# Optimization experiments

Hardware: AMD Instinct MI355X
Metric: run time of the kernel (lower is better)

Reference implementation:

```python
import jax, jax.numpy as jnp
import numpy as np

B, T, N, E = 4, 30, 2000, 32000
F_IN, F_HID, F_GRU, N_CLS = 8, 64, 128, 2


def setup_inputs() -> dict:
    key = jax.random.key(0)
    ks = jax.random.split(key, 12)
    return {
        "x": jax.random.normal(ks[0], (B, T, N, F_IN), jnp.float32),
        "edge_index": jax.random.randint(ks[1], (B, T, 2, E), 0, N, jnp.int32),
        "W1": jax.random.normal(ks[2], (F_IN, F_HID), jnp.float32) * 0.1,
        "b1": jax.random.normal(ks[3], (F_HID,), jnp.float32) * 0.1,
        "W2": jax.random.normal(ks[4], (F_HID, F_HID), jnp.float32) * 0.1,
        "b2": jax.random.normal(ks[5], (F_HID,), jnp.float32) * 0.1,
        "W_ih": jax.random.normal(ks[6], (3 * F_GRU, F_HID), jnp.float32) * 0.1,
        "W_hh": jax.random.normal(ks[7], (3 * F_GRU, F_GRU), jnp.float32) * 0.1,
        "b_ih": jax.random.normal(ks[8], (3 * F_GRU,), jnp.float32) * 0.1,
        "b_hh": jax.random.normal(ks[9], (3 * F_GRU,), jnp.float32) * 0.1,
        "fc_w": jax.random.normal(ks[10], (N_CLS, F_GRU), jnp.float32) * 0.1,
        "fc_b": jax.random.normal(ks[11], (N_CLS,), jnp.float32) * 0.1,
    }


def _gcn_conv(x, src, dst, W, b):
    # PyG GCNConv (edge_weight=None): add self-loops, sym-normalize, x@W, scatter-add, +bias
    n = x.shape[0]
    loops = jnp.arange(n, dtype=src.dtype)
    s = jnp.concatenate([src, loops])
    d = jnp.concatenate([dst, loops])
    deg = jax.ops.segment_sum(jnp.ones(s.shape[0], x.dtype), d, num_segments=n)
    dis = jnp.where(deg > 0, jax.lax.rsqrt(deg), 0.0)
    norm = dis[s] * dis[d]                      # [E+N]
    h = x @ W                                   # [N, Fout]
    msg = h[s] * norm[:, None]                  # gather + scale
    return jax.ops.segment_sum(msg, d, num_segments=n) + b


def _frame_embed(x, ei, W1, b1, W2, b2):
    # one graph frame -> mean-pooled 64-d embedding
    src, dst = ei[0], ei[1]
    h = jax.nn.relu(_gcn_conv(x, src, dst, W1, b1))
    h = jax.nn.relu(_gcn_conv(h, src, dst, W2, b2))
    return h.mean(axis=0)


def _gru(H, W_ih, W_hh, b_ih, b_hh):
    # H: [T, B, F_HID]; torch GRU gate order: r, z, n
    def step(h, x_t):
        gi = x_t @ W_ih.T + b_ih                # [B, 3H]
        gh = h @ W_hh.T + b_hh
        i_r, i_z, i_n = jnp.split(gi, 3, axis=-1)
        h_r, h_z, h_n = jnp.split(gh, 3, axis=-1)
        r = jax.nn.sigmoid(i_r + h_r)
        z = jax.nn.sigmoid(i_z + h_z)
        n = jnp.tanh(i_n + r * h_n)
        h_new = (1.0 - z) * n + z * h
        return h_new, None
    h0 = jnp.zeros((H.shape[1], F_GRU), H.dtype)
    h_final, _ = jax.lax.scan(step, h0, H)
    return h_final                              # [B, F_GRU]


def reference(x, edge_index, W1, b1, W2, b2, W_ih, W_hh, b_ih, b_hh, fc_w, fc_b):
    G = B * T
    xf = x.reshape(G, N, F_IN)
    eif = edge_index.reshape(G, 2, E)
    emb = jax.vmap(_frame_embed, in_axes=(0, 0, None, None, None, None))(
        xf, eif, W1, b1, W2, b2)                # [G, 64]
    H = emb.reshape(B, T, F_HID).transpose(1, 0, 2)  # [T, B, 64]
    h_final = _gru(H, W_ih, W_hh, b_ih, b_hh)   # [B, 128]
    return h_final @ fc_w.T + fc_b              # [B, 2]
```

## Files before the change

kernel.cpp:

```cpp
#include <hip/hip_runtime.h>
#include <math.h>

#define G    120
#define Nn   2000
#define Ee   32000
#define Tt   30
#define Bb   4
#define Fg   128
#define QCAP 9216
#define TSLOT 48

static __device__ __forceinline__ unsigned short f2bf(float f) {
    unsigned u = __float_as_uint(f);
    u += 0x7fffu + ((u >> 16) & 1u);
    return (unsigned short)(u >> 16);
}

#if defined(__has_builtin)
#if __has_builtin(__builtin_amdgcn_cvt_f32_fp8) && __has_builtin(__builtin_amdgcn_cvt_pk_fp8_f32)
#define HW_FP8 1
#endif
#if __has_builtin(__builtin_amdgcn_cvt_pk_f32_fp8)
#define HW_FP8_PK 1
typedef float floatx2 __attribute__((ext_vector_type(2)));
#endif
#endif

static __device__ __forceinline__ unsigned fp8_enc_sw(float x) {
    unsigned s = (__float_as_uint(x) >> 24) & 0x80u;
    float ax = fminf(fabsf(x), 448.f);
    unsigned em;
    if (ax < 0.015625f) {
        em = (unsigned)__float2int_rn(ax * 512.f);
    } else {
        int e = (int)(__float_as_uint(ax) >> 23) - 127;
        float r = ax * __uint_as_float((unsigned)((130 - e) << 23));
        int q = __float2int_rn(r);
        em = (unsigned)(((e + 7) << 3) + (q - 8));
        em = min(em, 126u);
    }
    return s | em;
}
static __device__ __forceinline__ float fp8_dec_sw(unsigned b) {
    unsigned em = b & 0x7fu;
    float mag;
    if (em < 8u) mag = (float)em * 0.001953125f;
    else mag = __uint_as_float((((em >> 3) + 120u) << 23) | ((em & 7u) << 20));
    return (b & 0x80u) ? -mag : mag;
}
static __device__ __forceinline__ unsigned fp8_pack4(float a, float b, float c, float d) {
#ifdef HW_FP8
    int w = __builtin_amdgcn_cvt_pk_fp8_f32(a, b, 0, false);
    w = __builtin_amdgcn_cvt_pk_fp8_f32(c, d, w, true);
    return (unsigned)w;
#else
    return fp8_enc_sw(a) | (fp8_enc_sw(b) << 8) | (fp8_enc_sw(c) << 16) | (fp8_enc_sw(d) << 24);
#endif
}
static __device__ __forceinline__ void fp8x4_dec(unsigned dw, float* o) {
#ifdef HW_FP8_PK
    floatx2 lo = __builtin_amdgcn_cvt_pk_f32_fp8((int)dw, false);
    floatx2 hi = __builtin_amdgcn_cvt_pk_f32_fp8((int)dw, true);
    o[0] = lo[0]; o[1] = lo[1]; o[2] = hi[0]; o[3] = hi[1];
#else
    o[0] = fp8_dec_sw(dw & 0xffu);
    o[1] = fp8_dec_sw((dw >> 8) & 0xffu);
    o[2] = fp8_dec_sw((dw >> 16) & 0xffu);
    o[3] = fp8_dec_sw((dw >> 24) & 0xffu);
#endif
}

__global__ void __launch_bounds__(1024, 1)
k_build(const int* __restrict__ ei, float* __restrict__ dis,
        int* __restrict__ startA, int* __restrict__ cntA,
        int* __restrict__ csr, unsigned* __restrict__ ellT,
        int* __restrict__ cntS, int* __restrict__ ordS,
        float* __restrict__ emb) {
    __shared__ int   hist[Nn];
    __shared__ float disl[Nn];
    __shared__ int   ws[512];
    __shared__ int   csr_l[QCAP];
    __shared__ int   cntQ[500];
    __shared__ int   exQ[500];
    __shared__ int   nodeAt[500];
    __shared__ int   dh[64];
    __shared__ int   db[64];
    __shared__ int   ovfS;
    int i = blockIdx.x;
    int xcd = i & 7;
    int j = i >> 3;
    int f15 = j >> 2;
    int q = j & 3;
    int g = xcd * 15 + f15;
    int gq = g * 4 + q;
    int lo = q * 500;
    int tid = threadIdx.x;
    for (int idx = tid; idx < Nn; idx += 1024) hist[idx] = 0;
    if (tid < 64) dh[tid] = 0;
    if (tid == 0) ovfS = 0;
    if (q == 0 && tid < 64) emb[g * 64 + tid] = 0.f;
    __syncthreads();
    const int* srcp = ei + (size_t)g * 2 * Ee;
    const int* dstp = srcp + Ee;
    for (int it = tid; it < Ee / 4; it += 1024) {
        int4 d = reinterpret_cast<const int4*>(dstp)[it];
        atomicAdd(&hist[d.x], 1);
        atomicAdd(&hist[d.y], 1);
        atomicAdd(&hist[d.z], 1);
        atomicAdd(&hist[d.w], 1);
    }
    __syncthreads();
    for (int idx = tid; idx < Nn; idx += 1024) disl[idx] = rsqrtf((float)hist[idx] + 1.0f);
    int cnt = 0;
    if (tid < 512) ws[tid] = (tid < 500) ? hist[lo + tid] : 0;
    if (tid < 500) cnt = hist[lo + tid];
    __syncthreads();
    for (int off = 1; off < 512; off <<= 1) {
        int v = 0;
        if (tid < 512 && tid >= off) v = ws[tid - off];
        __syncthreads();
        if (tid < 512) ws[tid] += v;
        __syncthreads();
    }
    int ex = 0;
    if (tid < 500) ex = ws[tid] - cnt;
    if (tid < 500) {
        hist[lo + tid] = ex;
        cntQ[tid] = cnt;
        exQ[tid] = ex;
        if (cnt > TSLOT - 1) atomicMax(&ovfS, 1);
        atomicAdd(&dh[min(cnt, 63)], 1);
    }
    __syncthreads();
    if (tid == 0) {
        int s = 0;
        for (int b = 0; b < 64; ++b) { db[b] = s; s += dh[b]; }
    }
    __syncthreads();
    if (tid < 64) dh[tid] = db[tid];
    __syncthreads();
    if (tid < 500) {
        int p = atomicAdd(&dh[min(cnt, 63)], 1);
        nodeAt[p] = tid;
    }
    for (int it = tid; it < Ee / 4; it += 1024) {
        int4 d = reinterpret_cast<const int4*>(dstp)[it];
        int4 s = reinterpret_cast<const int4*>(srcp)[it];
        if (d.x >= lo && d.x < lo + 500) { int p = atomicAdd(&hist[d.x], 1); if (p < QCAP) csr_l[p] = s.x; }
        if (d.y >= lo && d.y < lo + 500) { int p = atomicAdd(&hist[d.y], 1); if (p < QCAP) csr_l[p] = s.y; }
        if (d.z >= lo && d.z < lo + 500) { int p = atomicAdd(&hist[d.z], 1); if (p < QCAP) csr_l[p] = s.z; }
        if (d.w >= lo && d.w < lo + 500) { int p = atomicAdd(&hist[d.w], 1); if (p < QCAP) csr_l[p] = s.w; }
    }
    __syncthreads();
    if (tid < 500) {
        int n_own = lo + tid;
        size_t gn_own = (size_t)g * Nn + n_own;
        cntA[gn_own] = cnt;
        startA[gn_own] = gq * QCAP + ex;
        dis[gn_own] = disl[n_own];
        int sl = nodeAt[tid];
        int n2 = lo + sl;
        int cnt2 = cntQ[sl];
        int ex2 = exQ[sl];
        int c = q * 500 + tid;
        size_t gc = (size_t)g * Nn + c;
        cntS[gc] = cnt2;
        ordS[gc] = n2;
        float dn2 = disl[n2];
        unsigned* et = ellT + (size_t)g * TSLOT * Nn + c;
        et[0] = (unsigned)n2 | ((unsigned)f2bf(dn2 * dn2) << 16);
        int m2 = min(cnt2, TSLOT - 1);
        for (int e = 0; e < m2; ++e) {
            int s = csr_l[ex2 + e];
            et[(size_t)(e + 1) * Nn] = (unsigned)s | ((unsigned)f2bf(disl[s] * dn2) << 16);
        }
    }
    __syncthreads();
    if (ovfS) {
        int total = ws[511];
        int* cg = csr + (size_t)gq * QCAP;
        for (int it = tid; it < total; it += 1024) cg[it] = csr_l[it];
    }
}

__global__ void __launch_bounds__(256)
k_fused(const float* __restrict__ x, const unsigned* __restrict__ ellT,
        const int* __restrict__ cntS, const int* __restrict__ ordS,
        const int* __restrict__ startA, const int* __restrict__ csr,
        const float* __restrict__ dis,
        const float* __restrict__ W1, const float* __restrict__ b1,
        const float* __restrict__ W2, unsigned char* __restrict__ t2f) {
    int i = blockIdx.x;
    int xcd = i & 7;
    int j = i >> 3;
    int g = xcd * 15 + (j >> 3);
    int blk = j & 7;
    int p = blk * 256 + threadIdx.x;
    bool valid = (p < Nn);
    size_t gp = (size_t)g * Nn + (valid ? p : 0);
    int n = valid ? ordS[gp] : 0;
    int cnt = valid ? cntS[gp] : 0;
    int myc = valid ? (min(cnt, TSLOT - 1) + 1) : 0;
    float aX[8];
#pragma unroll
    for (int k = 0; k < 8; ++k) aX[k] = 0.f;
    {
        const unsigned* et = ellT + (size_t)g * TSLOT * Nn + (valid ? p : 0);
        const float4* x4 = reinterpret_cast<const float4*>(x + (size_t)g * Nn * 8);
        for (int e = 0; e < TSLOT; ++e) {
            if (!__any(e < myc)) break;
            if (e < myc) {
                unsigned u = et[(size_t)e * Nn];
                float w = __uint_as_float(u & 0xffff0000u);
                int s = u & 0xffffu;
                float4 r0 = x4[s * 2], r1 = x4[s * 2 + 1];
                aX[0] += r0.x * w; aX[1] += r0.y * w; aX[2] += r0.z * w; aX[3] += r0.w * w;
                aX[4] += r1.x * w; aX[5] += r1.y * w; aX[6] += r1.z * w; aX[7] += r1.w * w;
            }
        }
        if (cnt > TSLOT - 1) {
            size_t gn = (size_t)g * Nn + n;
            float dn = dis[gn];
            int start = startA[gn];
            const float* dsg = dis + (size_t)g * Nn;
            for (int e = TSLOT - 1; e < cnt; ++e) {
                int s = csr[start + e];
                float w = dsg[s] * dn;
                float4 r0 = x4[s * 2], r1 = x4[s * 2 + 1];
                aX[0] += r0.x * w; aX[1] += r0.y * w; aX[2] += r0.z * w; aX[3] += r0.w * w;
                aX[4] += r1.x * w; aX[5] += r1.y * w; aX[6] += r1.z * w; aX[7] += r1.w * w;
            }
        }
    }
    float h1r[64];
    {
        const float4* b14 = reinterpret_cast<const float4*>(b1);
#pragma unroll
        for (int f4 = 0; f4 < 16; ++f4) {
            float4 b = b14[f4];
            h1r[4 * f4 + 0] = b.x; h1r[4 * f4 + 1] = b.y;
            h1r[4 * f4 + 2] = b.z; h1r[4 * f4 + 3] = b.w;
        }
        const float4* W14 = reinterpret_cast<const float4*>(W1);
#pragma unroll
        for (int k = 0; k < 8; ++k) {
            float hk = aX[k];
#pragma unroll
            for (int f4 = 0; f4 < 16; ++f4) {
                float4 w = W14[k * 16 + f4];
                h1r[4 * f4 + 0] += hk * w.x; h1r[4 * f4 + 1] += hk * w.y;
                h1r[4 * f4 + 2] += hk * w.z; h1r[4 * f4 + 3] += hk * w.w;
            }
        }
#pragma unroll
        for (int f = 0; f < 64; ++f) h1r[f] = fmaxf(h1r[f], 0.f);
    }
    uint4 oh[2][2];
    {
        const float4* W24 = reinterpret_cast<const float4*>(W2);
#pragma unroll
        for (int hf = 0; hf < 2; ++hf) {
            float acch[32];
#pragma unroll
            for (int f = 0; f < 32; ++f) acch[f] = 0.f;
#pragma unroll
            for (int k = 0; k < 64; ++k) {
                float hk = h1r[k];
#pragma unroll
                for (int f4 = 0; f4 < 8; ++f4) {
                    float4 w = W24[k * 16 + hf * 8 + f4];
                    acch[4 * f4 + 0] += hk * w.x; acch[4 * f4 + 1] += hk * w.y;
                    acch[4 * f4 + 2] += hk * w.z; acch[4 * f4 + 3] += hk * w.w;
                }
            }
            oh[hf][0].x = fp8_pack4(acch[0],  acch[1],  acch[2],  acch[3]);
            oh[hf][0].y = fp8_pack4(acch[4],  acch[5],  acch[6],  acch[7]);
            oh[hf][0].z = fp8_pack4(acch[8],  acch[9],  acch[10], acch[11]);
            oh[hf][0].w = fp8_pack4(acch[12], acch[13], acch[14], acch[15]);
            oh[hf][1].x = fp8_pack4(acch[16], acch[17], acch[18], acch[19]);
            oh[hf][1].y = fp8_pack4(acch[20], acch[21], acch[22], acch[23]);
            oh[hf][1].z = fp8_pack4(acch[24], acch[25], acch[26], acch[27]);
            oh[hf][1].w = fp8_pack4(acch[28], acch[29], acch[30], acch[31]);
        }
    }
    if (valid) {
        uint4* op = reinterpret_cast<uint4*>(t2f + ((size_t)g * Nn + n) * 64);
        op[0] = oh[0][0]; op[1] = oh[0][1]; op[2] = oh[1][0]; op[3] = oh[1][1];
    }
}

__global__ void __launch_bounds__(1024, 1)
k_aggF(const unsigned char* __restrict__ t2f, const unsigned* __restrict__ ellT,
       const int* __restrict__ cntS, const int* __restrict__ ordS,
       const int* __restrict__ startA, const int* __restrict__ csr,
       const float* __restrict__ dis, const float* __restrict__ bias,
       float* __restrict__ emb) {
    __shared__ uint4 stage[Nn * 5];
    int i = blockIdx.x;
    int xcd = i & 7;
    int j = i >> 3;
    int g = xcd * 15 + (j >> 1);
    int half = j & 1;
    int tid = threadIdx.x;
    int w = tid >> 6, lane = tid & 63;
    {
        const uint4* src = reinterpret_cast<const uint4*>(t2f + (size_t)g * Nn * 64);
        for (int it = tid; it < Nn * 4; it += 1024)
            stage[(it >> 2) * 5 + (it & 3)] = src[it];
    }
    __syncthreads();
#define ROWFMA(dw, base) { float o_[4]; fp8x4_dec(dw, o_); \
    acc[base + 0] += o_[0] * wt; acc[base + 1] += o_[1] * wt; \
    acc[base + 2] += o_[2] * wt; acc[base + 3] += o_[3] * wt; }
    int po = w * 64 + lane;
    int p = half * 1000 + po;
    bool valid = (po < 1000);
    size_t gp = (size_t)g * Nn + (valid ? p : 0);
    int cnt = valid ? cntS[gp] : 0;
    int myc = valid ? (min(cnt, TSLOT - 1) + 1) : 0;
    float acc[64];
#pragma unroll
    for (int k = 0; k < 64; ++k) acc[k] = 0.f;
    const unsigned* et = ellT + (size_t)g * TSLOT * Nn + (valid ? p : 0);
    for (int e = 0; e < TSLOT; ++e) {
        if (!__any(e < myc)) break;
        if (e < myc) {
            unsigned u = et[(size_t)e * Nn];
            float wt = __uint_as_float(u & 0xffff0000u);
            int s = u & 0xffffu;
            uint4 r0 = stage[s * 5], r1 = stage[s * 5 + 1];
            uint4 r2 = stage[s * 5 + 2], r3 = stage[s * 5 + 3];
            ROWFMA(r0.x, 0)  ROWFMA(r0.y, 4)  ROWFMA(r0.z, 8)  ROWFMA(r0.w, 12)
            ROWFMA(r1.x, 16) ROWFMA(r1.y, 20) ROWFMA(r1.z, 24) ROWFMA(r1.w, 28)
            ROWFMA(r2.x, 32) ROWFMA(r2.y, 36) ROWFMA(r2.z, 40) ROWFMA(r2.w, 44)
            ROWFMA(r3.x, 48) ROWFMA(r3.y, 52) ROWFMA(r3.z, 56) ROWFMA(r3.w, 60)
        }
    }
    if (cnt > TSLOT - 1) {
        int n = ordS[gp];
        size_t gn = (size_t)g * Nn + n;
        float dn = dis[gn];
        int start = startA[gn];
        const float* dsg = dis + (size_t)g * Nn;
        for (int e = TSLOT - 1; e < cnt; ++e) {
            int s = csr[start + e];
            float wt = dsg[s] * dn;
            uint4 r0 = stage[s * 5], r1 = stage[s * 5 + 1];
            uint4 r2 = stage[s * 5 + 2], r3 = stage[s * 5 + 3];
            ROWFMA(r0.x, 0)  ROWFMA(r0.y, 4)  ROWFMA(r0.z, 8)  ROWFMA(r0.w, 12)
            ROWFMA(r1.x, 16) ROWFMA(r1.y, 20) ROWFMA(r1.z, 24) ROWFMA(r1.w, 28)
            ROWFMA(r2.x, 32) ROWFMA(r2.y, 36) ROWFMA(r2.z, 40) ROWFMA(r2.w, 44)
            ROWFMA(r3.x, 48) ROWFMA(r3.y, 52) ROWFMA(r3.z, 56) ROWFMA(r3.w, 60)
        }
    }
#undef ROWFMA
    float pool = 0.f;
#pragma unroll
    for (int k = 0; k < 64; ++k) {
        float v = valid ? fmaxf(acc[k] + bias[k], 0.f) : 0.f;
        v += __shfl_xor(v, 1);  v += __shfl_xor(v, 2);  v += __shfl_xor(v, 4);
        v += __shfl_xor(v, 8);  v += __shfl_xor(v, 16); v += __shfl_xor(v, 32);
        if (lane == k) pool = v;
    }
    atomicAdd(&emb[g * 64 + lane], pool * (1.0f / Nn));
}

__global__ void k_gi(const float* __restrict__ emb, const float* __restrict__ W_ih,
                     const float* __restrict__ b_ih, float* __restrict__ gi) {
    __shared__ float xs[64];
    int g = blockIdx.x;
    int j = threadIdx.x;
    if (j < 64) xs[j] = emb[g * 64 + j];
    __syncthreads();
    float a0 = 0.f, a1 = 0.f, a2 = 0.f, a3 = 0.f;
    const float* wr = W_ih + j * 64;
#pragma unroll
    for (int k = 0; k < 16; ++k) {
        a0 += wr[4 * k + 0] * xs[4 * k + 0];
        a1 += wr[4 * k + 1] * xs[4 * k + 1];
        a2 += wr[4 * k + 2] * xs[4 * k + 2];
        a3 += wr[4 * k + 3] * xs[4 * k + 3];
    }
    gi[(size_t)g * 384 + j] = b_ih[j] + ((a0 + a1) + (a2 + a3));
}

__global__ void __launch_bounds__(768, 1)
k_gru_seq(const float* __restrict__ gi, const float* __restrict__ W_hh,
          const float* __restrict__ b_hh, const float* __restrict__ fc_w,
          const float* __restrict__ fc_b, float* __restrict__ out) {
    __shared__ float h[Fg];
    __shared__ float part[768];
    int b = blockIdx.x;
    int tid = threadIdx.x;
    int row = tid >> 1;
    int half = tid & 1;
    float w[64];
    const float* wr = W_hh + (size_t)row * Fg + half * 64;
#pragma unroll
    for (int i = 0; i < 64; ++i) w[i] = wr[i];
    if (tid < Fg) h[tid] = 0.f;
    __syncthreads();
    for (int t = 0; t < Tt; ++t) {
        const float* hh = &h[half * 64];
        float a0 = 0.f, a1 = 0.f, a2 = 0.f, a3 = 0.f;
#pragma unroll
        for (int i = 0; i < 16; ++i) {
            a0 += w[4 * i + 0] * hh[4 * i + 0];
            a1 += w[4 * i + 1] * hh[4 * i + 1];
            a2 += w[4 * i + 2] * hh[4 * i + 2];
            a3 += w[4 * i + 3] * hh[4 * i + 3];
        }
        part[tid] = (a0 + a1) + (a2 + a3);
        __syncthreads();
        if (tid < Fg) {
            int j = tid;
            const float* gib = gi + ((size_t)b * Tt + t) * 384;
            float hr = b_hh[j]       + part[2 * j]           + part[2 * j + 1];
            float hz = b_hh[128 + j] + part[2 * (128 + j)]   + part[2 * (128 + j) + 1];
            float hn = b_hh[256 + j] + part[2 * (256 + j)]   + part[2 * (256 + j) + 1];
            float r  = 1.f / (1.f + expf(-(gib[j] + hr)));
            float z  = 1.f / (1.f + expf(-(gib[128 + j] + hz)));
            float nn = tanhf(gib[256 + j] + r * hn);
            h[j] = (1.f - z) * nn + z * h[j];
        }
        __syncthreads();
    }
    if (tid < 2) {
        float acc = fc_b[tid];
        for (int k = 0; k < Fg; ++k) acc += fc_w[tid * Fg + k] * h[k];
        out[b * 2 + tid] = acc;
    }
}

extern "C" void kernel_launch(void* const* d_in, const int* in_sizes, int n_in,
                              void* d_out, int out_size, void* d_ws, size_t ws_size,
                              hipStream_t stream) {
    const float* x     = (const float*)d_in[0];
    const int*   ei    = (const int*)  d_in[1];
    const float* W1    = (const float*)d_in[2];
    const float* b1    = (const float*)d_in[3];
    const float* W2    = (const float*)d_in[4];
    const float* b2    = (const float*)d_in[5];
    const float* W_ih  = (const float*)d_in[6];
    const float* W_hh  = (const float*)d_in[7];
    const float* b_ih  = (const float*)d_in[8];
    const float* b_hh  = (const float*)d_in[9];
    const float* fc_w  = (const float*)d_in[10];
    const float* fc_b  = (const float*)d_in[11];
    float* out = (float*)d_out;

    char* ws = (char*)d_ws;
    size_t off = 0;
    auto alloc = [&](size_t bytes) -> void* {
        void* p = ws + off;
        off = (off + bytes + 255) & ~(size_t)255;
        return p;
    };
    float*    dis    = (float*)   alloc((size_t)G * Nn * 4);
    int*      startA = (int*)     alloc((size_t)G * Nn * 4);
    int*      cntA   = (int*)     alloc((size_t)G * Nn * 4);
    int*      cntS   = (int*)     alloc((size_t)G * Nn * 4);
    int*      ordS   = (int*)     alloc((size_t)G * Nn * 4);
    int*      csr    = (int*)     alloc((size_t)G * 4 * QCAP * 4);
    unsigned* ellT   = (unsigned*)alloc((size_t)G * TSLOT * Nn * 4);
    unsigned char* t2f = (unsigned char*)alloc((size_t)G * Nn * 64);
    float*    emb    = (float*)   alloc((size_t)G * 64 * 4);
    float*    gi     = (float*)   alloc((size_t)G * 384 * 4);
    (void)ws_size; (void)in_sizes; (void)n_in; (void)out_size;

    hipLaunchKernelGGL(k_build,   dim3(480), dim3(1024), 0, stream, ei, dis, startA, cntA, csr, ellT, cntS, ordS, emb);
    hipLaunchKernelGGL(k_fused,   dim3(960), dim3(256), 0, stream, x, ellT, cntS, ordS, startA, csr, dis, W1, b1, W2, t2f);
    hipLaunchKernelGGL(k_aggF,    dim3(240), dim3(1024), 0, stream, t2f, ellT, cntS, ordS, startA, csr, dis, b2, emb);
    hipLaunchKernelGGL(k_gi,      dim3(G), dim3(384), 0, stream, emb, W_ih, b_ih, gi);
    hipLaunchKernelGGL(k_gru_seq, dim3(Bb), dim3(768), 0, stream, gi, W_hh, b_hh, fc_w, fc_b, out);
}
```

Before: 263.3 us.

## Split k_fused output features across two blocks and stream layer-1 in chunks

k_fused now launches twice as many blocks, each computing one 32-wide half of the layer-2 output per node. Layer-1 hidden values are produced in 8-wide chunks and fed straight into the layer-2 accumulation, so the full 64-float hidden vector never has to stay in registers. Launch bounds request 8 blocks per SM. The aim is lower register pressure and higher occupancy, at the cost of doing the edge gather and layer-1 matmul twice per node.

```diff
diff --git a/kernel.cpp b/kernel.cpp
--- a/kernel.cpp
+++ b/kernel.cpp
@@ -183,7 +183,7 @@
     }
 }
 
-__global__ void __launch_bounds__(256)
+__global__ void __launch_bounds__(256, 8)
 k_fused(const float* __restrict__ x, const unsigned* __restrict__ ellT,
         const int* __restrict__ cntS, const int* __restrict__ ordS,
         const int* __restrict__ startA, const int* __restrict__ csr,
@@ -193,8 +193,9 @@
     int i = blockIdx.x;
     int xcd = i & 7;
     int j = i >> 3;
-    int g = xcd * 15 + (j >> 3);
-    int blk = j & 7;
+    int g = xcd * 15 + (j >> 4);
+    int blk = (j >> 1) & 7;
+    int hf = j & 1;
     int p = blk * 256 + threadIdx.x;
     bool valid = (p < Nn);
     size_t gp = (size_t)g * Nn + (valid ? p : 0);
@@ -232,60 +233,56 @@
             }
         }
     }
-    float h1r[64];
+    float acc[32];
+#pragma unroll
+    for (int f = 0; f < 32; ++f) acc[f] = 0.f;
     {
+        const float4* W14 = reinterpret_cast<const float4*>(W1);
         const float4* b14 = reinterpret_cast<const float4*>(b1);
-#pragma unroll
-        for (int f4 = 0; f4 < 16; ++f4) {
-            float4 b = b14[f4];
-            h1r[4 * f4 + 0] = b.x; h1r[4 * f4 + 1] = b.y;
-            h1r[4 * f4 + 2] = b.z; h1r[4 * f4 + 3] = b.w;
-        }
-        const float4* W14 = reinterpret_cast<const float4*>(W1);
-#pragma unroll
-        for (int k = 0; k < 8; ++k) {
-            float hk = aX[k];
-#pragma unroll
-            for (int f4 = 0; f4 < 16; ++f4) {
-                float4 w = W14[k * 16 + f4];
-                h1r[4 * f4 + 0] += hk * w.x; h1r[4 * f4 + 1] += hk * w.y;
-                h1r[4 * f4 + 2] += hk * w.z; h1r[4 * f4 + 3] += hk * w.w;
+        const float4* W24h = reinterpret_cast<const float4*>(W2) + hf * 8;
+#pragma unroll
+        for (int c = 0; c < 8; ++c) {
+            float h1c[8];
+            {
+                float4 ba = b14[c * 2 + 0], bb = b14[c * 2 + 1];
+                h1c[0] = ba.x; h1c[1] = ba.y; h1c[2] = ba.z; h1c[3] = ba.w;
+                h1c[4] = bb.x; h1c[5] = bb.y; h1c[6] = bb.z; h1c[7] = bb.w;
             }
-        }
-#pragma unroll
-        for (int f = 0; f < 64; ++f) h1r[f] = fmaxf(h1r[f], 0.f);
-    }
-    uint4 oh[2][2];
-    {
-        const float4* W24 = reinterpret_cast<const float4*>(W2);
-#pragma unroll
-        for (int hf = 0; hf < 2; ++hf) {
-            float acch[32];
-#pragma unroll
-            for (int f = 0; f < 32; ++f) acch[f] = 0.f;
-#pragma unroll
-            for (int k = 0; k < 64; ++k) {
-                float hk = h1r[k];
+#pragma unroll
+            for (int k = 0; k < 8; ++k) {
+                float hk = aX[k];
+                float4 wa = W14[k * 16 + c * 2 + 0];
+                float4 wb = W14[k * 16 + c * 2 + 1];
+                h1c[0] += hk * wa.x; h1c[1] += hk * wa.y;
+                h1c[2] += hk * wa.z; h1c[3] += hk * wa.w;
+                h1c[4] += hk * wb.x; h1c[5] += hk * wb.y;
+                h1c[6] += hk * wb.z; h1c[7] += hk * wb.w;
+            }
+#pragma unroll
+            for (int u = 0; u < 8; ++u) {
+                float hk = fmaxf(h1c[u], 0.f);
 #pragma unroll
                 for (int f4 = 0; f4 < 8; ++f4) {
-                    float4 w = W24[k * 16 + hf * 8 + f4];
-                    acch[4 * f4 + 0] += hk * w.x; acch[4 * f4 + 1] += hk * w.y;
-                    acch[4 * f4 + 2] += hk * w.z; acch[4 * f4 + 3] += hk * w.w;
+                    float4 w = W24h[(c * 8 + u) * 16 + f4];
+                    acc[4 * f4 + 0] += hk * w.x; acc[4 * f4 + 1] += hk * w.y;
+                    acc[4 * f4 + 2] += hk * w.z; acc[4 * f4 + 3] += hk * w.w;
                 }
             }
-            oh[hf][0].x = fp8_pack4(acch[0],  acch[1],  acch[2],  acch[3]);
-            oh[hf][0].y = fp8_pack4(acch[4],  acch[5],  acch[6],  acch[7]);
-            oh[hf][0].z = fp8_pack4(acch[8],  acch[9],  acch[10], acch[11]);
-            oh[hf][0].w = fp8_pack4(acch[12], acch[13], acch[14], acch[15]);
-            oh[hf][1].x = fp8_pack4(acch[16], acch[17], acch[18], acch[19]);
-            oh[hf][1].y = fp8_pack4(acch[20], acch[21], acch[22], acch[23]);
-            oh[hf][1].z = fp8_pack4(acch[24], acch[25], acch[26], acch[27]);
-            oh[hf][1].w = fp8_pack4(acch[28], acch[29], acch[30], acch[31]);
-        }
-    }
+        }
+    }
+    uint4 o0, o1;
+    o0.x = fp8_pack4(acc[0],  acc[1],  acc[2],  acc[3]);
+    o0.y = fp8_pack4(acc[4],  acc[5],  acc[6],  acc[7]);
+    o0.z = fp8_pack4(acc[8],  acc[9],  acc[10], acc[11]);
+    o0.w = fp8_pack4(acc[12], acc[13], acc[14], acc[15]);
+    o1.x = fp8_pack4(acc[16], acc[17], acc[18], acc[19]);
+    o1.y = fp8_pack4(acc[20], acc[21], acc[22], acc[23]);
+    o1.z = fp8_pack4(acc[24], acc[25], acc[26], acc[27]);
+    o1.w = fp8_pack4(acc[28], acc[29], acc[30], acc[31]);
     if (valid) {
         uint4* op = reinterpret_cast<uint4*>(t2f + ((size_t)g * Nn + n) * 64);
-        op[0] = oh[0][0]; op[1] = oh[0][1]; op[2] = oh[1][0]; op[3] = oh[1][1];
+        op[hf * 2 + 0] = o0;
+        op[hf * 2 + 1] = o1;
     }
 }
 
@@ -469,7 +466,7 @@
     (void)ws_size; (void)in_sizes; (void)n_in; (void)out_size;
 
     hipLaunchKernelGGL(k_build,   dim3(480), dim3(1024), 0, stream, ei, dis, startA, cntA, csr, ellT, cntS, ordS, emb);
-    hipLaunchKernelGGL(k_fused,   dim3(960), dim3(256), 0, stream, x, ellT, cntS, ordS, startA, csr, dis, W1, b1, W2, t2f);
+    hipLaunchKernelGGL(k_fused,   dim3(1920), dim3(256), 0, stream, x, ellT, cntS, ordS, startA, csr, dis, W1, b1, W2, t2f);
     hipLaunchKernelGGL(k_aggF,    dim3(240), dim3(1024), 0, stream, t2f, ellT, cntS, ordS, startA, csr, dis, b2, emb);
     hipLaunchKernelGGL(k_gi,      dim3(G), dim3(384), 0, stream, emb, W_ih, b_ih, gi);
     hipLaunchKernelGGL(k_gru_seq, dim3(Bb), dim3(768), 0, stream, gi, W_hh, b_hh, fc_w, fc_b, out);
```

Result: slower. 326.5 us (+24.0%).
